# Optimization experiments

Hardware: AMD Instinct MI355X
Metric: run time of the kernel (lower is better)

Reference implementation:

```python
import jax, jax.numpy as jnp
import numpy as np

OUT_H, OUT_W = 7, 7
SCALE = 0.25
SR = 2  # sampling_ratio


def _prep(c, size):
    # mmcv bilinear_interpolate index/weight logic (aligned edge handling)
    c0 = jnp.maximum(c, 0.0)
    low = jnp.floor(c0).astype(jnp.int32)
    hi = low >= size - 1
    low = jnp.where(hi, size - 1, low)
    high = jnp.where(hi, size - 1, low + 1)
    c0 = jnp.where(hi, low.astype(c.dtype), c0)
    frac = c0 - low.astype(c.dtype)
    return low, high, frac


def _roi_align(feat, rois):
    B, C, H, W = feat.shape
    N = rois.shape[0]
    bidx = rois[:, 0].astype(jnp.int32)
    off = 0.5  # aligned=True
    sx = rois[:, 1] * SCALE - off
    sy = rois[:, 2] * SCALE - off
    ex = rois[:, 3] * SCALE - off
    ey = rois[:, 4] * SCALE - off
    bw = (ex - sx) / OUT_W  # bin sizes [N]
    bh = (ey - sy) / OUT_H
    sub = (jnp.arange(SR, dtype=feat.dtype) + 0.5) / SR  # sub-sample offsets in a bin
    # sample coordinates: [N, OUT, SR]
    ys = sy[:, None, None] + (jnp.arange(OUT_H, dtype=feat.dtype)[None, :, None] + sub[None, None, :]) * bh[:, None, None]
    xs = sx[:, None, None] + (jnp.arange(OUT_W, dtype=feat.dtype)[None, :, None] + sub[None, None, :]) * bw[:, None, None]
    vy = (ys > -1.0) & (ys < H)
    vx = (xs > -1.0) & (xs < W)
    ylo, yhi, ly = _prep(ys, H)
    xlo, xhi, lx = _prep(xs, W)
    bb = bidx[:, None, None, None, None]

    def gather(yi, xi):
        # -> [N, OUT_H, SR, OUT_W, SR, C]
        return feat[bb, :, yi[:, :, :, None, None], xi[:, None, None, :, :]]

    ly5 = ly[:, :, :, None, None, None]
    lx5 = lx[:, None, None, :, :, None]
    val = (gather(ylo, xlo) * (1 - ly5) * (1 - lx5)
           + gather(ylo, xhi) * (1 - ly5) * lx5
           + gather(yhi, xlo) * ly5 * (1 - lx5)
           + gather(yhi, xhi) * ly5 * lx5)
    valid = (vy[:, :, :, None, None] & vx[:, None, None, :, :])[..., None]
    val = jnp.where(valid, val, 0.0)
    out = val.sum(axis=(2, 4)) / (SR * SR)  # avg over sampling grid -> [N, OUT_H, OUT_W, C]
    return jnp.transpose(out, (0, 3, 1, 2))  # [N, C, OUT_H, OUT_W]


def setup_inputs() -> dict:
    key = jax.random.key(0)
    k1, k2, k3, k4, k5, k6 = jax.random.split(key, 6)
    B, C, H, W = 2, 256, 200, 336
    N = 1000
    feat = jax.random.normal(k1, (B, C, H, W), dtype=jnp.float32)
    img_w, img_h = W / SCALE, H / SCALE  # rois are in image coordinates
    bidx = jax.random.randint(k2, (N,), 0, B).astype(jnp.float32)
    x1 = jax.random.uniform(k3, (N,), minval=0.0, maxval=img_w - 32.0)
    y1 = jax.random.uniform(k4, (N,), minval=0.0, maxval=img_h - 32.0)
    bw = jax.random.uniform(k5, (N,), minval=16.0, maxval=320.0)
    bh = jax.random.uniform(k6, (N,), minval=16.0, maxval=320.0)
    x2 = jnp.minimum(x1 + bw, img_w - 1.0)
    y2 = jnp.minimum(y1 + bh, img_h - 1.0)
    rois = jnp.stack([bidx, x1, y1, x2, y2], axis=1).astype(jnp.float32)
    return {"feat": feat, "rois": rois}


def reference(feat, rois):
    return _roi_align(feat, rois)
```

## Files before the change

### kernel.cpp

```cpp
#include <hip/hip_runtime.h>
#include <hip/hip_fp16.h>

#define POOL 7
#define NBIN 49
#define SP_SCALE 0.25f

constexpr int Cc = 256, Hc = 200, Wc = 336;
constexpr int HWc = Hc * Wc;

__global__ __launch_bounds__(256) void transpose_f16_kernel(
    const float* __restrict__ in, __half* __restrict__ outp) {
  __shared__ float tile[32][33];
  int b  = blockIdx.z;
  int p0 = blockIdx.x * 32;
  int c0 = blockIdx.y * 32;
  const float* src = in   + (size_t)b * Cc * HWc;
  __half*      dst = outp + (size_t)b * Cc * HWc;
  int tx = threadIdx.x;
  int ty = threadIdx.y;

  float4 v = *(const float4*)(src + (size_t)(c0 + ty) * HWc + p0 + tx * 4);
  tile[ty][tx * 4 + 0] = v.x;
  tile[ty][tx * 4 + 1] = v.y;
  tile[ty][tx * 4 + 2] = v.z;
  tile[ty][tx * 4 + 3] = v.w;
  __syncthreads();
  union { __half h[4]; uint2 u; } o;
  o.h[0] = __float2half(tile[tx * 4 + 0][ty]);
  o.h[1] = __float2half(tile[tx * 4 + 1][ty]);
  o.h[2] = __float2half(tile[tx * 4 + 2][ty]);
  o.h[3] = __float2half(tile[tx * 4 + 3][ty]);
  *(uint2*)(dst + (size_t)(p0 + ty) * Cc + c0 + tx * 4) = o.u;
}

__global__ __launch_bounds__(256, 4) void gather_kernel(
    const __half* __restrict__ ft, const float* __restrict__ rois,
    float* __restrict__ out, int N) {
  int T  = N * NBIN;
  int nb = (T + 7) >> 3;
  int j = blockIdx.x;
  int q = nb >> 3, rr = nb & 7;
  int xc = j & 7, loc = j >> 3;
  int blk = (xc < rr ? xc * (q + 1) : rr * (q + 1) + (xc - rr) * q) + loc;

  int sub = threadIdx.x & 31;
  int bl  = threadIdx.x >> 5;
  int w = blk * 8 + bl;
  if (w >= T) return;
  int bin = w % NBIN;
  int n   = w / NBIN;
  int ph  = bin / POOL, pw = bin % POOL;

  const float* r = rois + (size_t)n * 5;
  int   bidx = (int)r[0];
  float sx = fmaf(r[1], SP_SCALE, -0.5f);
  float sy = fmaf(r[2], SP_SCALE, -0.5f);
  float bw = (fmaf(r[3], SP_SCALE, -0.5f) - sx) * (1.0f / POOL);
  float bh = (fmaf(r[4], SP_SCALE, -0.5f) - sy) * (1.0f / POOL);

  int   rows[4]; float wy[4];
#pragma unroll
  for (int i = 0; i < 2; ++i) {
    float y = sy + ((float)ph + 0.25f + 0.5f * (float)i) * bh;
    bool v = (y > -1.0f) && (y < (float)Hc);
    float y0 = fmaxf(y, 0.0f);
    int lo = (int)y0;
    int hi;
    if (lo >= Hc - 1) { lo = Hc - 1; hi = Hc - 1; y0 = (float)lo; }
    else              { hi = lo + 1; }
    float f = y0 - (float)lo;
    rows[i * 2]     = lo; rows[i * 2 + 1] = hi;
    wy[i * 2]       = v ? (1.0f - f) * 0.25f : 0.0f;
    wy[i * 2 + 1]   = v ? f * 0.25f : 0.0f;
  }
  int   cols[4]; float wx[4];
#pragma unroll
  for (int i = 0; i < 2; ++i) {
    float x = sx + ((float)pw + 0.25f + 0.5f * (float)i) * bw;
    bool v = (x > -1.0f) && (x < (float)Wc);
    float x0 = fmaxf(x, 0.0f);
    int lo = (int)x0;
    int hi;
    if (lo >= Wc - 1) { lo = Wc - 1; hi = Wc - 1; x0 = (float)lo; }
    else              { hi = lo + 1; }
    float f = x0 - (float)lo;
    cols[i * 2]     = lo; cols[i * 2 + 1] = hi;
    wx[i * 2]       = v ? (1.0f - f) : 0.0f;
    wx[i * 2 + 1]   = v ? f : 0.0f;
  }

  const __half* fp = ft + (size_t)bidx * HWc * Cc + sub * 8;

  uint4 v[16];
#pragma unroll
  for (int rI = 0; rI < 4; ++rI) {
    const __half* rp = fp + (size_t)rows[rI] * (Wc * Cc);
#pragma unroll
    for (int cI = 0; cI < 4; ++cI)
      v[rI * 4 + cI] = *(const uint4*)(rp + (size_t)cols[cI] * Cc);
  }

  float a0 = 0.f, a1 = 0.f, a2 = 0.f, a3 = 0.f;
  float a4 = 0.f, a5 = 0.f, a6 = 0.f, a7 = 0.f;
#pragma unroll
  for (int k = 0; k < 16; ++k) {
    float wk = wy[k >> 2] * wx[k & 3];
    union { uint4 u; __half2 h2[4]; } t;
    t.u = v[k];
    float2 f0 = __half22float2(t.h2[0]);
    float2 f1 = __half22float2(t.h2[1]);
    float2 f2 = __half22float2(t.h2[2]);
    float2 f3 = __half22float2(t.h2[3]);
    a0 = fmaf(wk, f0.x, a0); a1 = fmaf(wk, f0.y, a1);
    a2 = fmaf(wk, f1.x, a2); a3 = fmaf(wk, f1.y, a3);
    a4 = fmaf(wk, f2.x, a4); a5 = fmaf(wk, f2.y, a5);
    a6 = fmaf(wk, f3.x, a6); a7 = fmaf(wk, f3.y, a7);
  }

  float* op = out + ((size_t)n * Cc + (size_t)sub * 8) * NBIN + bin;
  op[0]        = a0;
  op[NBIN]     = a1;
  op[2 * NBIN] = a2;
  op[3 * NBIN] = a3;
  op[4 * NBIN] = a4;
  op[5 * NBIN] = a5;
  op[6 * NBIN] = a6;
  op[7 * NBIN] = a7;
}

__global__ __launch_bounds__(256) void roi_align_fallback(
    const float* __restrict__ feat, const float* __restrict__ rois,
    float* __restrict__ out, int N) {
  long long idx = (long long)blockIdx.x * blockDim.x + threadIdx.x;
  long long total = (long long)N * Cc * NBIN;
  if (idx >= total) return;
  int pw = (int)(idx % POOL);
  int ph = (int)((idx / POOL) % POOL);
  int c  = (int)((idx / NBIN) % Cc);
  int n  = (int)(idx / ((long long)NBIN * Cc));
  const float* r = rois + (size_t)n * 5;
  int   b  = (int)r[0];
  float sx = fmaf(r[1], SP_SCALE, -0.5f);
  float sy = fmaf(r[2], SP_SCALE, -0.5f);
  float bw = (fmaf(r[3], SP_SCALE, -0.5f) - sx) * (1.0f / POOL);
  float bh = (fmaf(r[4], SP_SCALE, -0.5f) - sy) * (1.0f / POOL);
  const float* fp = feat + ((size_t)b * Cc + c) * (size_t)HWc;
  float acc = 0.0f;
#pragma unroll
  for (int iy = 0; iy < 2; ++iy) {
    float y = sy + ((float)ph + 0.25f + 0.5f * iy) * bh;
    bool vy = (y > -1.0f) && (y < (float)Hc);
    float y0 = fmaxf(y, 0.0f);
    int ylo = (int)y0, yhi;
    if (ylo >= Hc - 1) { ylo = Hc - 1; yhi = Hc - 1; y0 = (float)ylo; }
    else               { yhi = ylo + 1; }
    float ly = y0 - (float)ylo;
#pragma unroll
    for (int ix = 0; ix < 2; ++ix) {
      float x = sx + ((float)pw + 0.25f + 0.5f * ix) * bw;
      bool vx = (x > -1.0f) && (x < (float)Wc);
      float x0 = fmaxf(x, 0.0f);
      int xlo = (int)x0, xhi;
      if (xlo >= Wc - 1) { xlo = Wc - 1; xhi = Wc - 1; x0 = (float)xlo; }
      else               { xhi = xlo + 1; }
      float lx = x0 - (float)xlo;
      if (vy && vx) {
        float v00 = fp[(size_t)ylo * Wc + xlo];
        float v01 = fp[(size_t)ylo * Wc + xhi];
        float v10 = fp[(size_t)yhi * Wc + xlo];
        float v11 = fp[(size_t)yhi * Wc + xhi];
        acc += v00 * (1.0f - ly) * (1.0f - lx) + v01 * (1.0f - ly) * lx
             + v10 * ly * (1.0f - lx) + v11 * ly * lx;
      }
    }
  }
  out[idx] = acc * 0.25f;
}

extern "C" void kernel_launch(void* const* d_in, const int* in_sizes, int n_in,
                              void* d_out, int out_size, void* d_ws, size_t ws_size,
                              hipStream_t stream) {
  const float* feat = (const float*)d_in[0];
  const float* rois = (const float*)d_in[1];
  float* out = (float*)d_out;
  const int N = in_sizes[1] / 5;
  (void)n_in; (void)out_size;

  size_t need = (size_t)2 * Cc * HWc * sizeof(__half);
  if (ws_size >= need) {
    __half* ft = (__half*)d_ws;
    dim3 tb(8, 32);
    dim3 tg(HWc / 32, Cc / 32, 2);
    transpose_f16_kernel<<<tg, tb, 0, stream>>>(feat, ft);
    int T = N * NBIN;
    int nb = (T + 7) / 8;
    gather_kernel<<<nb, 256, 0, stream>>>(ft, rois, out, N);
  } else {
    long long total = (long long)N * Cc * NBIN;
    roi_align_fallback<<<(int)((total + 255) / 256), 256, 0, stream>>>(feat, rois, out, N);
  }
}
```

Baseline: 90.50 us.

## Sort ROIs by batch and Morton-ordered center to improve gather locality

Adds a single-block bitonic sort kernel that orders ROIs by batch index and a Z-order code of their spatial center. The gather kernel then walks ROIs in that order, so ROIs processed close together in time hit nearby feature rows and reuse cached lines. It also drops the min-blocks-per-CU launch bound on the gather kernel. The cost is an extra serial 1024-thread kernel launch with many barriers, plus an indirect load per warp.

```diff
diff --git a/kernel.cpp b/kernel.cpp
--- a/kernel.cpp
+++ b/kernel.cpp
@@ -7,6 +7,40 @@
 
 constexpr int Cc = 256, Hc = 200, Wc = 336;
 constexpr int HWc = Hc * Wc;
+
+__global__ __launch_bounds__(1024) void sort_rois_kernel(
+    const float* __restrict__ rois, int N, unsigned int* __restrict__ order) {
+  __shared__ unsigned int k[1024];
+  int t = threadIdx.x;
+  unsigned int key = 0xFFFFFFFFu;
+  if (t < N) {
+    const float* r = rois + (size_t)t * 5;
+    int b = (int)r[0];
+    float cx = (r[1] + r[3]) * 0.5f * SP_SCALE;
+    float cy = (r[2] + r[4]) * 0.5f * SP_SCALE;
+    int qx = min(31, max(0, (int)(cx * (32.0f / (float)Wc))));
+    int qy = min(31, max(0, (int)(cy * (32.0f / (float)Hc))));
+    unsigned int m = 0;
+#pragma unroll
+    for (int i = 0; i < 5; ++i)
+      m |= (((qy >> i) & 1u) << (2 * i + 1)) | (((qx >> i) & 1u) << (2 * i));
+    key = ((unsigned int)b << 20) | (m << 10) | (unsigned int)t;
+  }
+  k[t] = key;
+  __syncthreads();
+  for (int size = 2; size <= 1024; size <<= 1) {
+    for (int stride = size >> 1; stride > 0; stride >>= 1) {
+      int j = t ^ stride;
+      if (j > t) {
+        unsigned int a = k[t], c = k[j];
+        bool up = ((t & size) == 0);
+        if ((a > c) == up) { k[t] = c; k[j] = a; }
+      }
+      __syncthreads();
+    }
+  }
+  order[t] = k[t];
+}
 
 __global__ __launch_bounds__(256) void transpose_f16_kernel(
     const float* __restrict__ in, __half* __restrict__ outp) {
@@ -33,9 +67,9 @@
   *(uint2*)(dst + (size_t)(p0 + ty) * Cc + c0 + tx * 4) = o.u;
 }
 
-__global__ __launch_bounds__(256, 4) void gather_kernel(
+__global__ __launch_bounds__(256) void gather_kernel(
     const __half* __restrict__ ft, const float* __restrict__ rois,
-    float* __restrict__ out, int N) {
+    float* __restrict__ out, int N, const unsigned int* __restrict__ order) {
   int T  = N * NBIN;
   int nb = (T + 7) >> 3;
   int j = blockIdx.x;
@@ -48,7 +82,8 @@
   int w = blk * 8 + bl;
   if (w >= T) return;
   int bin = w % NBIN;
-  int n   = w / NBIN;
+  int ns  = w / NBIN;
+  int n   = order ? (int)(order[ns] & 1023u) : ns;
   int ph  = bin / POOL, pw = bin % POOL;
 
   const float* r = rois + (size_t)n * 5;
@@ -186,15 +221,24 @@
   const int N = in_sizes[1] / 5;
   (void)n_in; (void)out_size;
 
-  size_t need = (size_t)2 * Cc * HWc * sizeof(__half);
+  size_t ft_bytes = (size_t)2 * Cc * HWc * sizeof(__half);
+  size_t need = ft_bytes + 4096;
   if (ws_size >= need) {
     __half* ft = (__half*)d_ws;
+    unsigned int* order = (unsigned int*)((char*)d_ws + ft_bytes);
+
+    bool use_sort = (N <= 1024);
+    if (use_sort)
+      sort_rois_kernel<<<1, 1024, 0, stream>>>(rois, N, order);
+
     dim3 tb(8, 32);
     dim3 tg(HWc / 32, Cc / 32, 2);
     transpose_f16_kernel<<<tg, tb, 0, stream>>>(feat, ft);
+
     int T = N * NBIN;
     int nb = (T + 7) / 8;
-    gather_kernel<<<nb, 256, 0, stream>>>(ft, rois, out, N);
+    gather_kernel<<<nb, 256, 0, stream>>>(ft, rois, out, N,
+                                          use_sort ? order : nullptr);
   } else {
     long long total = (long long)N * Cc * NBIN;
     roi_align_fallback<<<(int)((total + 255) / 256), 256, 0, stream>>>(feat, rois, out, N);
```

Result: slower. 92.67 us (+2.4%).
